# Kernel optimization log

Hardware: AMD Instinct MI355X
Metric: run time of the kernel (lower is better)

Reference implementation:

```python
import jax, jax.numpy as jnp
import numpy as np

N_GENES = 8192      # input genes
WM = 4              # width_multiplier: hidden nodes per gene
HID = N_GENES * WM  # 32768 hidden units
N_TF = 1024         # embedding dim (TF activities)
GPT = 64            # target genes per TF in the prior network
BATCH = 256
EPS = 1e-5          # BatchNorm1d eps


def _connectivity():
    # layer1: hidden node h belongs to gene h // WM (fan_in = 1)
    rows1 = np.arange(HID, dtype=np.int32)
    cols1 = (rows1 // WM).astype(np.int32)
    # layer2: fully connected within each gene group (WM x WM blocks)
    rows2 = np.repeat(np.arange(HID, dtype=np.int32), WM)
    cols2 = (((np.arange(HID)[:, None] // WM) * WM) + np.arange(WM)).astype(np.int32).ravel()
    # layer3: each TF connects to all WM nodes of GPT randomly chosen genes
    rng = np.random.default_rng(0)
    genes = rng.integers(0, N_GENES, size=(N_TF, GPT))
    cols3 = (genes[:, :, None] * WM + np.arange(WM)).astype(np.int32).reshape(-1)
    rows3 = np.repeat(np.arange(N_TF, dtype=np.int32), GPT * WM)
    return rows1, cols1, rows2, cols2, rows3, cols3


def _sparse_linear(x, w, b, rows, cols, out_dim):
    # y[b, o] = sum_{e: rows[e]==o} w[e] * x[b, cols[e]] + b[o]
    xe = x[:, cols] * w  # [B, E]
    y = jnp.zeros((x.shape[0], out_dim), x.dtype).at[:, rows].add(xe)
    return y + b


def _batchnorm(x):
    # BatchNorm1d(affine=False), training mode: biased batch var
    m = jnp.mean(x, axis=0)
    v = jnp.var(x, axis=0)
    return (x - m) / jnp.sqrt(v + EPS)


def setup_inputs() -> dict:
    key = jax.random.key(0)
    k = jax.random.split(key, 7)
    rows1, cols1, rows2, cols2, rows3, cols3 = _connectivity()
    inp = {
        "features": jax.random.normal(k[0], (BATCH, N_GENES), jnp.float32),
        "w1": jax.random.normal(k[1], (HID,), jnp.float32),                 # fan_in 1
        "b1": jax.random.normal(k[2], (HID,), jnp.float32) * 0.01,
        "w2": jax.random.normal(k[3], (HID * WM,), jnp.float32) / np.sqrt(WM),
        "b2": jax.random.normal(k[4], (HID,), jnp.float32) * 0.01,
        "w3": jax.random.normal(k[5], (N_TF * GPT * WM,), jnp.float32) / np.sqrt(GPT * WM),
        "b3": jax.random.normal(k[6], (N_TF,), jnp.float32) * 0.01,
        "rows1": jnp.asarray(rows1), "cols1": jnp.asarray(cols1),
        "rows2": jnp.asarray(rows2), "cols2": jnp.asarray(cols2),
        "rows3": jnp.asarray(rows3), "cols3": jnp.asarray(cols3),
    }
    return inp


def reference(features, w1, b1, w2, b2, w3, b3,
              rows1, cols1, rows2, cols2, rows3, cols3):
    h = _sparse_linear(features, w1, b1, rows1, cols1, HID)
    h = _batchnorm(jax.nn.relu(h))
    h = _sparse_linear(h, w2, b2, rows2, cols2, HID)
    h = _batchnorm(jax.nn.relu(h))
    z = _sparse_linear(h, w3, b3, rows3, cols3, N_TF)
    return _batchnorm(z)
```

## Files before the change

kernel.cpp:

```cpp
#include <hip/hip_runtime.h>
#include <cstddef>

#define EPS 1e-5f

constexpr int NG  = 8192;
constexpr int HID = 32768;
constexpr int NTF = 1024;
constexpr int B   = 256;

static __device__ __forceinline__ unsigned short f2bf(float v) {
    union { float f; unsigned u; } a; a.f = v;
    unsigned r = a.u + 0x7fffu + ((a.u >> 16) & 1u);
    return (unsigned short)(r >> 16);
}

__global__ __launch_bounds__(256) void fused12(
    const float* __restrict__ x,
    const float* __restrict__ w1,
    const float* __restrict__ b1,
    const float* __restrict__ w2,
    const float* __restrict__ b2,
    unsigned short* __restrict__ h2rT,
    float* __restrict__ m2g,
    float* __restrict__ inv2g)
{
    const int lane  = threadIdx.x & 63;
    const int slice = threadIdx.x >> 6;
    const int c     = (blockIdx.x << 6) + lane;
    const int g     = c >> 2;
    const int b0    = slice << 6;

    __shared__ float redA[4][64], redB[4][64];
    __shared__ float m1s[64], inv1s[64];

    const float w1c = w1[c], b1c = b1[c];
    const float* xp = x + (size_t)b0 * NG + g;

    float s = 0.f, s2 = 0.f;
    #pragma unroll 8
    for (int i = 0; i < 64; ++i) {
        float h = fmaxf(fmaf(w1c, xp[(size_t)i * NG], b1c), 0.f);
        s += h;
        s2 = fmaf(h, h, s2);
    }
    redA[slice][lane] = s;
    redB[slice][lane] = s2;
    __syncthreads();
    if (slice == 0) {
        float S  = redA[0][lane] + redA[1][lane] + redA[2][lane] + redA[3][lane];
        float S2 = redB[0][lane] + redB[1][lane] + redB[2][lane] + redB[3][lane];
        float m  = S * (1.f / 256.f);
        float v  = fmaf(-m, m, S2 * (1.f / 256.f));
        m1s[lane]   = m;
        inv1s[lane] = rsqrtf(v + EPS);
    }
    __syncthreads();

    const int lbase = lane & ~3;
    const int gbase = g << 2;
    float w1j[4], b1j[4], w2s[4];
    float bconst = b2[c];
    #pragma unroll
    for (int j = 0; j < 4; ++j) {
        w1j[j] = w1[gbase + j];
        b1j[j] = b1[gbase + j];
        float wv = w2[(c << 2) + j] * inv1s[lbase + j];
        w2s[j] = wv;
        bconst = fmaf(-wv, m1s[lbase + j], bconst);
    }

    float t2s = 0.f, t2s2 = 0.f;
    unsigned short* op = h2rT + (size_t)c * B + b0;
    for (int i0 = 0; i0 < 64; i0 += 4) {
        ushort4 pk;
        unsigned short* pp = (unsigned short*)&pk;
        #pragma unroll
        for (int u = 0; u < 4; ++u) {
            float v = xp[(size_t)(i0 + u) * NG];
            float acc = bconst;
            #pragma unroll
            for (int j = 0; j < 4; ++j) {
                float r = fmaxf(fmaf(w1j[j], v, b1j[j]), 0.f);
                acc = fmaf(w2s[j], r, acc);
            }
            float r2 = fmaxf(acc, 0.f);
            t2s += r2;
            t2s2 = fmaf(r2, r2, t2s2);
            pp[u] = f2bf(r2);
        }
        *(ushort4*)(op + i0) = pk;
    }

    __syncthreads();
    redA[slice][lane] = t2s;
    redB[slice][lane] = t2s2;
    __syncthreads();
    if (slice == 0) {
        float S  = redA[0][lane] + redA[1][lane] + redA[2][lane] + redA[3][lane];
        float S2 = redB[0][lane] + redB[1][lane] + redB[2][lane] + redB[3][lane];
        float m  = S * (1.f / 256.f);
        float v  = fmaf(-m, m, S2 * (1.f / 256.f));
        m2g[c]   = m;
        inv2g[c] = rsqrtf(v + EPS);
    }
}

__global__ __launch_bounds__(256) void fused3(
    const unsigned short* __restrict__ h2,
    const float* __restrict__ m2g,
    const float* __restrict__ inv2g,
    const float* __restrict__ w3,
    const float* __restrict__ b3,
    const int*   __restrict__ cols3,
    float* __restrict__ out)
{
    const int t   = blockIdx.x;
    const int tid = threadIdx.x;

    __shared__ float wls[256];
    __shared__ int   als[256];
    __shared__ float wred[4], rs[4], rs2[4];
    __shared__ float accq[4][256];

    int   col = cols3[(t << 8) + tid];
    float wv  = w3[(t << 8) + tid] * inv2g[col];
    wls[tid]  = wv;
    als[tid]  = col << 9;
    float bp  = wv * m2g[col];
    #pragma unroll
    for (int o = 32; o > 0; o >>= 1) bp += __shfl_xor(bp, o);
    if ((tid & 63) == 0) wred[tid >> 6] = bp;
    __syncthreads();

    const int q    = tid >> 6;
    const int lane = tid & 63;
    const int roff = lane << 3;
    const char* h2c = (const char*)h2;
    float a0 = 0.f, a1 = 0.f, a2 = 0.f, a3 = 0.f;
    #pragma unroll 8
    for (int e2 = 0; e2 < 64; ++e2) {
        const int e = (e2 << 2) | q;
        float w = wls[e];
        uint2 u = *(const uint2*)(h2c + als[e] + roff);
        union { unsigned v; float f; } p0, p1, p2, p3;
        p0.v = u.x << 16;
        p1.v = u.x & 0xffff0000u;
        p2.v = u.y << 16;
        p3.v = u.y & 0xffff0000u;
        a0 = fmaf(w, p0.f, a0);
        a1 = fmaf(w, p1.f, a1);
        a2 = fmaf(w, p2.f, a2);
        a3 = fmaf(w, p3.f, a3);
    }
    *(float4*)&accq[q][lane << 2] = make_float4(a0, a1, a2, a3);
    __syncthreads();

    const float zbias = b3[t] - (wred[0] + wred[1] + wred[2] + wred[3]);
    float z = accq[0][tid] + accq[1][tid] + accq[2][tid] + accq[3][tid] + zbias;

    float s = z, s2 = z * z;
    #pragma unroll
    for (int o = 32; o > 0; o >>= 1) {
        s  += __shfl_xor(s, o);
        s2 += __shfl_xor(s2, o);
    }
    if ((tid & 63) == 0) { rs[tid >> 6] = s; rs2[tid >> 6] = s2; }
    __syncthreads();
    float S  = rs[0] + rs[1] + rs[2] + rs[3];
    float S2 = rs2[0] + rs2[1] + rs2[2] + rs2[3];
    float m  = S * (1.f / 256.f);
    float v  = fmaf(-m, m, S2 * (1.f / 256.f));
    float invs = rsqrtf(v + EPS);
    out[(size_t)tid * NTF + t] = (z - m) * invs;
}

extern "C" void kernel_launch(void* const* d_in, const int* in_sizes, int n_in,
                              void* d_out, int out_size, void* d_ws, size_t ws_size,
                              hipStream_t stream) {
    const float* x   = (const float*)d_in[0];
    const float* w1  = (const float*)d_in[1];
    const float* b1  = (const float*)d_in[2];
    const float* w2  = (const float*)d_in[3];
    const float* b2  = (const float*)d_in[4];
    const float* w3  = (const float*)d_in[5];
    const float* b3  = (const float*)d_in[6];
    const int* cols3 = (const int*)d_in[12];
    float* out = (float*)d_out;

    unsigned short* h2rT = (unsigned short*)d_ws;
    float* m2g   = (float*)(h2rT + (size_t)HID * B);
    float* inv2g = m2g + HID;

    fused12<<<HID / 64, 256, 0, stream>>>(x, w1, b1, w2, b2, h2rT, m2g, inv2g);
    fused3<<<NTF, 256, 0, stream>>>(h2rT, m2g, inv2g, w3, b3, cols3, out);
}
```

Before: 116.5 us.

## Store h2 in batch-slice-major blocks and gather contiguous gene groups in layer 3

The bf16 intermediate is now written as [4 batch slices][HID][64], so the four hidden nodes of one gene sit together as 512 contiguous bytes per slice. The layer-3 kernel gathers 16-byte chunks across 32 lanes per gene group and loops over the batch slices, reducing partial sums through shared memory. The goal is fully coalesced gather reads for the per-TF sparse sum. In exchange it adds several extra block barriers and shared-memory reduction passes per slice.

```diff
diff --git a/kernel.cpp b/kernel.cpp
--- a/kernel.cpp
+++ b/kernel.cpp
@@ -20,7 +20,7 @@
     const float* __restrict__ b1,
     const float* __restrict__ w2,
     const float* __restrict__ b2,
-    unsigned short* __restrict__ h2rT,
+    unsigned short* __restrict__ h2b,
     float* __restrict__ m2g,
     float* __restrict__ inv2g)
 {
@@ -70,7 +70,7 @@
     }
 
     float t2s = 0.f, t2s2 = 0.f;
-    unsigned short* op = h2rT + (size_t)c * B + b0;
+    unsigned short* op = h2b + ((size_t)slice * HID + c) * 64;
     for (int i0 = 0; i0 < 64; i0 += 4) {
         ushort4 pk;
         unsigned short* pp = (unsigned short*)&pk;
@@ -118,45 +118,63 @@
     const int tid = threadIdx.x;
 
     __shared__ float wls[256];
-    __shared__ int   als[256];
+    __shared__ int   als[64];
     __shared__ float wred[4], rs[4], rs2[4];
-    __shared__ float accq[4][256];
+    __shared__ float accq[32][64];
+    __shared__ float red2[4][64];
+    __shared__ float zs[256];
 
     int   col = cols3[(t << 8) + tid];
     float wv  = w3[(t << 8) + tid] * inv2g[col];
     wls[tid]  = wv;
-    als[tid]  = col << 9;
+    if (tid < 64) als[tid] = cols3[(t << 8) + (tid << 2)] << 7;
     float bp  = wv * m2g[col];
     #pragma unroll
     for (int o = 32; o > 0; o >>= 1) bp += __shfl_xor(bp, o);
     if ((tid & 63) == 0) wred[tid >> 6] = bp;
     __syncthreads();
 
-    const int q    = tid >> 6;
-    const int lane = tid & 63;
-    const int roff = lane << 3;
-    const char* h2c = (const char*)h2;
-    float a0 = 0.f, a1 = 0.f, a2 = 0.f, a3 = 0.f;
-    #pragma unroll 8
-    for (int e2 = 0; e2 < 64; ++e2) {
-        const int e = (e2 << 2) | q;
-        float w = wls[e];
-        uint2 u = *(const uint2*)(h2c + als[e] + roff);
-        union { unsigned v; float f; } p0, p1, p2, p3;
-        p0.v = u.x << 16;
-        p1.v = u.x & 0xffff0000u;
-        p2.v = u.y << 16;
-        p3.v = u.y & 0xffff0000u;
-        a0 = fmaf(w, p0.f, a0);
-        a1 = fmaf(w, p1.f, a1);
-        a2 = fmaf(w, p2.f, a2);
-        a3 = fmaf(w, p3.f, a3);
-    }
-    *(float4*)&accq[q][lane << 2] = make_float4(a0, a1, a2, a3);
+    const char* h2c  = (const char*)h2;
+    const int   lrow = (tid & 7) << 3;
+
+    for (int bt = 0; bt < 4; ++bt) {
+        float a0=0.f,a1=0.f,a2=0.f,a3=0.f,a4=0.f,a5=0.f,a6=0.f,a7=0.f;
+        const char* bpt = h2c + (size_t)bt * ((size_t)HID * 128) + ((tid & 31) << 4);
+        #pragma unroll
+        for (int jb = 0; jb < 8; ++jb) {
+            const int   j = (jb << 3) + (tid >> 5);
+            const float w = wls[(jb << 5) + (tid >> 3)];
+            const uint4 u = *(const uint4*)(bpt + als[j]);
+            union { unsigned v; float f; } p0,p1,p2,p3,p4,p5,p6,p7;
+            p0.v = u.x << 16; p1.v = u.x & 0xffff0000u;
+            p2.v = u.y << 16; p3.v = u.y & 0xffff0000u;
+            p4.v = u.z << 16; p5.v = u.z & 0xffff0000u;
+            p6.v = u.w << 16; p7.v = u.w & 0xffff0000u;
+            a0 = fmaf(w, p0.f, a0); a1 = fmaf(w, p1.f, a1);
+            a2 = fmaf(w, p2.f, a2); a3 = fmaf(w, p3.f, a3);
+            a4 = fmaf(w, p4.f, a4); a5 = fmaf(w, p5.f, a5);
+            a6 = fmaf(w, p6.f, a6); a7 = fmaf(w, p7.f, a7);
+        }
+        __syncthreads();
+        *(float4*)&accq[tid >> 3][lrow]     = make_float4(a0, a1, a2, a3);
+        *(float4*)&accq[tid >> 3][lrow + 4] = make_float4(a4, a5, a6, a7);
+        __syncthreads();
+        {
+            const int r = tid & 63, gq = tid >> 6;
+            float p = 0.f;
+            #pragma unroll
+            for (int i = 0; i < 8; ++i) p += accq[(gq << 3) + i][r];
+            red2[gq][r] = p;
+        }
+        __syncthreads();
+        if (tid < 64)
+            zs[(bt << 6) + tid] = red2[0][tid] + red2[1][tid]
+                                + red2[2][tid] + red2[3][tid];
+    }
     __syncthreads();
 
     const float zbias = b3[t] - (wred[0] + wred[1] + wred[2] + wred[3]);
-    float z = accq[0][tid] + accq[1][tid] + accq[2][tid] + accq[3][tid] + zbias;
+    float z = zs[tid] + zbias;
 
     float s = z, s2 = z * z;
     #pragma unroll
@@ -187,10 +205,10 @@
     const int* cols3 = (const int*)d_in[12];
     float* out = (float*)d_out;
 
-    unsigned short* h2rT = (unsigned short*)d_ws;
-    float* m2g   = (float*)(h2rT + (size_t)HID * B);
+    unsigned short* h2b = (unsigned short*)d_ws;
+    float* m2g   = (float*)(h2b + (size_t)HID * B);
     float* inv2g = m2g + HID;
 
-    fused12<<<HID / 64, 256, 0, stream>>>(x, w1, b1, w2, b2, h2rT, m2g, inv2g);
-    fused3<<<NTF, 256, 0, stream>>>(h2rT, m2g, inv2g, w3, b3, cols3, out);
-}
+    fused12<<<HID / 64, 256, 0, stream>>>(x, w1, b1, w2, b2, h2b, m2g, inv2g);
+    fused3<<<NTF, 256, 0, stream>>>(h2b, m2g, inv2g, w3, b3, cols3, out);
+}
```

Result: no change. 117.4 us (+0.8%).
